# Kernel optimization log

Hardware: AMD Instinct MI355X
Metric: run time of the kernel (lower is better)

Reference implementation:

```python
import jax, jax.numpy as jnp
import numpy as np

D_MODEL = 1024
N_HEADS = 16
D_K = D_MODEL // N_HEADS
D_FF = 4096
EPS = 1e-5


def layer_norm(x, gamma, beta):
    mu = jnp.mean(x, axis=-1, keepdims=True)
    var = jnp.var(x, axis=-1, keepdims=True)
    return (x - mu) * jax.lax.rsqrt(var + EPS) * gamma + beta


def setup_inputs() -> dict:
    key = jax.random.key(0)
    ks = jax.random.split(key, 16)
    B, S = 4, 1024
    s = 0.02
    inp = {
        "x": jax.random.normal(ks[0], (B, S, D_MODEL), dtype=jnp.float32),
        "mask": jnp.ones((B, 1, 1, S), dtype=jnp.int32),
        "Wq": jax.random.normal(ks[1], (D_MODEL, D_MODEL), jnp.float32) * s,
        "bq": jnp.zeros((D_MODEL,), jnp.float32),
        "Wk": jax.random.normal(ks[2], (D_MODEL, D_MODEL), jnp.float32) * s,
        "bk": jnp.zeros((D_MODEL,), jnp.float32),
        "Wv": jax.random.normal(ks[3], (D_MODEL, D_MODEL), jnp.float32) * s,
        "bv": jnp.zeros((D_MODEL,), jnp.float32),
        "Wo": jax.random.normal(ks[4], (D_MODEL, D_MODEL), jnp.float32) * s,
        "bo": jnp.zeros((D_MODEL,), jnp.float32),
        "W1": jax.random.normal(ks[5], (D_MODEL, D_FF), jnp.float32) * s,
        "b1": jnp.zeros((D_FF,), jnp.float32),
        "W2": jax.random.normal(ks[6], (D_FF, D_MODEL), jnp.float32) * s,
        "b2": jnp.zeros((D_MODEL,), jnp.float32),
        "ln1_g": jnp.ones((D_MODEL,), jnp.float32),
        "ln1_b": jnp.zeros((D_MODEL,), jnp.float32),
        "ln2_g": jnp.ones((D_MODEL,), jnp.float32),
        "ln2_b": jnp.zeros((D_MODEL,), jnp.float32),
    }
    return inp


def reference(x, mask, Wq, bq, Wk, bk, Wv, bv, Wo, bo, W1, b1, W2, b2,
              ln1_g, ln1_b, ln2_g, ln2_b):
    B, S, _ = x.shape
    # QKV projections -> [B, H, S, d_k]
    def split_heads(t):
        return t.reshape(B, S, N_HEADS, D_K).transpose(0, 2, 1, 3)
    Q = split_heads(x @ Wq + bq)
    K = split_heads(x @ Wk + bk)
    V = split_heads(x @ Wv + bv)
    # scores [B, H, S, S]
    scores = jnp.einsum('bhqd,bhkd->bhqk', Q, K) / jnp.sqrt(jnp.float32(D_K))
    scores = jnp.where(mask == 0, jnp.float32(-1e9), scores)
    attn = jax.nn.softmax(scores, axis=-1)
    ctx = jnp.einsum('bhqk,bhkd->bhqd', attn, V)
    ctx = ctx.transpose(0, 2, 1, 3).reshape(B, S, D_MODEL)
    attn_out = ctx @ Wo + bo
    # residual + LN (dropout is identity in eval)
    h = layer_norm(x + attn_out, ln1_g, ln1_b)
    ff = jax.nn.relu(h @ W1 + b1) @ W2 + b2
    return layer_norm(h + ff, ln2_g, ln2_b)
```

## Files before the change

kernel.cpp:

```cpp
#include <hip/hip_runtime.h>
#include <hip/hip_bf16.h>

typedef __attribute__((ext_vector_type(8))) short bf16x8;
typedef __attribute__((ext_vector_type(4))) float f32x4;
typedef __attribute__((ext_vector_type(16))) float f32x16;
typedef unsigned int u32;
typedef unsigned short ush;

#define SEQ 1024
#define MTOT 4096
#define QSCALE_LOG2 0.18033688f

#if __has_builtin(__builtin_amdgcn_exp2f)
#define EXP2(x) __builtin_amdgcn_exp2f(x)
#else
#define EXP2(x) exp2f(x)
#endif

__device__ __forceinline__ ush f2bf(float f){
  u32 u = __float_as_uint(f);
  u32 r = (u + 0x7fffu + ((u >> 16) & 1u)) >> 16;
  return (ush)r;
}

__device__ __forceinline__ f32x4 mfma16(bf16x8 a, bf16x8 b, f32x4 c){
  return __builtin_amdgcn_mfma_f32_16x16x32_bf16(a, b, c, 0, 0, 0);
}
__device__ __forceinline__ f32x16 mfma32(bf16x8 a, bf16x8 b, f32x16 c){
  return __builtin_amdgcn_mfma_f32_32x32x16_bf16(a, b, c, 0, 0, 0);
}

__device__ __forceinline__ u32 cvtpk(float lo, float hi){
  u32 r; asm("v_cvt_pk_bf16_f32 %0, %1, %2" : "=v"(r) : "v"(lo), "v"(hi)); return r;
}

__device__ __forceinline__ void gload_lds16(const ush* g, ush* l){
  __builtin_amdgcn_global_load_lds(
      (const __attribute__((address_space(1))) u32*)g,
      (__attribute__((address_space(3))) u32*)l, 16, 0, 0);
}

__global__ __launch_bounds__(256) void cvt_kernel(const float* __restrict__ src,
                                                  ush* __restrict__ dst, int n){
  int i = (blockIdx.x * 256 + threadIdx.x) * 4;
  if (i < n){
    float4 v = *(const float4*)&src[i];
    ushort4 o = { f2bf(v.x), f2bf(v.y), f2bf(v.z), f2bf(v.w) };
    *(ushort4*)&dst[i] = o;
  }
}

__global__ __launch_bounds__(256) void tconv_kernel(const float* __restrict__ src,
                                                    ush* __restrict__ dst, int R, int C){
  __shared__ float t[32][33];
  int tx = threadIdx.x & 31, ty = threadIdx.x >> 5;
  int r0 = blockIdx.y * 32, c0 = blockIdx.x * 32;
  #pragma unroll
  for (int i = 0; i < 32; i += 8)
    t[ty + i][tx] = src[(size_t)(r0 + ty + i) * C + (c0 + tx)];
  __syncthreads();
  #pragma unroll
  for (int i = 0; i < 32; i += 8)
    dst[(size_t)(c0 + ty + i) * R + (r0 + tx)] = f2bf(t[tx][ty + i]);
}

__global__ __launch_bounds__(256) void biaspack_kernel(const float* __restrict__ bq,
    const float* __restrict__ bk, const float* __restrict__ bv, float* __restrict__ dst){
  int i = blockIdx.x * 256 + threadIdx.x;
  if (i < 3072){
    float v = (i < 1024) ? bq[i] : (i < 2048) ? bk[i - 1024] : bv[i - 2048];
    dst[i] = v;
  }
}

__global__ __launch_bounds__(256) void vtrans_kernel(const ush* __restrict__ qkv,
                                                     ush* __restrict__ VT){
  __shared__ ush t[32][34];
  int tx = threadIdx.x & 31, ty = threadIdx.x >> 5;
  int bh = blockIdx.z, b = bh >> 4, h = bh & 15;
  int k0 = blockIdx.x * 32, d0 = blockIdx.y * 32;
  #pragma unroll
  for (int i = 0; i < 32; i += 8)
    t[ty + i][tx] = qkv[(size_t)(b * SEQ + k0 + ty + i) * 3072 + 2048 + h * 64 + d0 + tx];
  __syncthreads();
  #pragma unroll
  for (int i = 0; i < 32; i += 8)
    VT[(size_t)(bh * 64 + d0 + ty + i) * SEQ + k0 + tx] = t[tx][ty + i];
}

__device__ __forceinline__ void stage_piece(ush* piece, const ush* g0, int K,
                                            int tid, int w){
  #pragma unroll
  for (int I = 0; I < 2; I++){
    int c = I * 512 + tid;
    int r = c >> 2;
    int gl = (c & 3) ^ ((r >> 1) & 3);
    gload_lds16(g0 + (size_t)r * K + gl * 8, piece + I * 4096 + w * 512);
  }
}

__device__ __forceinline__ bf16x8 frag(const ush* piece, int row, int g){
  int phys = g ^ ((row >> 1) & 3);
  return *(const bf16x8*)(piece + row * 32 + phys * 8);
}

#define PH_BAR_TOP() do{ __builtin_amdgcn_sched_barrier(0); \
  __builtin_amdgcn_s_barrier(); \
  asm volatile("s_waitcnt lgkmcnt(0)" ::: "memory"); \
  __builtin_amdgcn_sched_barrier(0); \
  __builtin_amdgcn_s_setprio(1); }while(0)
#define PH_BAR_BOT() do{ __builtin_amdgcn_s_setprio(0); \
  __builtin_amdgcn_sched_barrier(0); \
  __builtin_amdgcn_s_barrier(); }while(0)

template<int RELU, int OUTF32, int SCALEQ>
__global__ __launch_bounds__(512, 2) void gemm8_kernel(
    const ush* __restrict__ A, const ush* __restrict__ Bt,
    const float* __restrict__ bias,
    ush* __restrict__ Cb, float* __restrict__ Cf,
    int M, int N, int K, int ldc, int ksl)
{
  __shared__ ush lds[2][2][2][8192];
  const int tid = threadIdx.x;
  const int lane = tid & 63, w = tid >> 6;
  const int g = lane >> 4, qr = lane & 15;
  const int wr = w >> 2, wc = w & 3;
  const int gx = gridDim.x;
  const int nwg = gx * gridDim.y;
  const int id = blockIdx.y * gx + blockIdx.x;
  const int swz = (id & 7) * (nwg >> 3) + (id >> 3);
  const int bn = (swz % gx) * 256;
  const int bm = (swz / gx) * 256;
  const int kbase = blockIdx.z * ksl;
  const int NT = ksl >> 6;
  const ush* Ab = A  + (size_t)bm * K + kbase;
  const ush* Bb = Bt + (size_t)bn * K + kbase;

  stage_piece(lds[0][0][0], Ab,      K, tid, w);
  stage_piece(lds[0][1][0], Bb,      K, tid, w);
  stage_piece(lds[0][0][1], Ab + 32, K, tid, w);
  stage_piece(lds[0][1][1], Bb + 32, K, tid, w);
  if (NT > 1){
    stage_piece(lds[1][0][0], Ab + 64, K, tid, w);
    stage_piece(lds[1][1][0], Bb + 64, K, tid, w);
  }
  asm volatile("s_waitcnt vmcnt(4)" ::: "memory");
  __builtin_amdgcn_sched_barrier(0);
  __builtin_amdgcn_s_barrier();

  f32x4 acc[8][4] = {};
  const int ar = wr * 128 + qr;
  const int br = wc * 64 + qr;

  for (int T = 0; T < NT; ++T){
    const int cb = T & 1, nb = cb ^ 1;
    const ush* An = Ab + (size_t)(T + 1) * 64;
    const ush* Bn = Bb + (size_t)(T + 1) * 64;
    const ush* Af = Ab + (size_t)(T + 2) * 64;
    const ush* Bf = Bb + (size_t)(T + 2) * 64;
    bf16x8 af[4], bfr[4];

    #pragma unroll
    for (int j = 0; j < 4; j++) bfr[j] = frag(lds[cb][1][0], br + j * 16, g);
    #pragma unroll
    for (int i = 0; i < 4; i++) af[i] = frag(lds[cb][0][0], ar + i * 16, g);
    if (T + 1 < NT) stage_piece(lds[nb][0][1], An + 32, K, tid, w);
    PH_BAR_TOP();
    #pragma unroll
    for (int i = 0; i < 4; i++)
      #pragma unroll
      for (int j = 0; j < 4; j++)
        acc[i][j] = mfma16(af[i], bfr[j], acc[i][j]);
    PH_BAR_BOT();

    #pragma unroll
    for (int i = 0; i < 4; i++) af[i] = frag(lds[cb][0][0], ar + 64 + i * 16, g);
    if (T + 1 < NT) stage_piece(lds[nb][1][1], Bn + 32, K, tid, w);
    PH_BAR_TOP();
    #pragma unroll
    for (int i = 0; i < 4; i++)
      #pragma unroll
      for (int j = 0; j < 4; j++)
        acc[4 + i][j] = mfma16(af[i], bfr[j], acc[4 + i][j]);
    PH_BAR_BOT();

    #pragma unroll
    for (int j = 0; j < 4; j++) bfr[j] = frag(lds[cb][1][1], br + j * 16, g);
    #pragma unroll
    for (int i = 0; i < 4; i++) af[i] = frag(lds[cb][0][1], ar + i * 16, g);
    if (T + 2 < NT) stage_piece(lds[cb][0][0], Af, K, tid, w);
    PH_BAR_TOP();
    #pragma unroll
    for (int i = 0; i < 4; i++)
      #pragma unroll
      for (int j = 0; j < 4; j++)
        acc[i][j] = mfma16(af[i], bfr[j], acc[i][j]);
    PH_BAR_BOT();

    #pragma unroll
    for (int i = 0; i < 4; i++) af[i] = frag(lds[cb][0][1], ar + 64 + i * 16, g);
    if (T + 2 < NT) stage_piece(lds[cb][1][0], Bf, K, tid, w);
    PH_BAR_TOP();
    #pragma unroll
    for (int i = 0; i < 4; i++)
      #pragma unroll
      for (int j = 0; j < 4; j++)
        acc[4 + i][j] = mfma16(af[i], bfr[j], acc[4 + i][j]);
    __builtin_amdgcn_s_setprio(0);
    __builtin_amdgcn_sched_barrier(0);
    asm volatile("s_waitcnt vmcnt(4)" ::: "memory");
    __builtin_amdgcn_sched_barrier(0);
    __builtin_amdgcn_s_barrier();
  }

  float* Cfz = Cf;
  if (OUTF32) Cfz = Cf + (size_t)blockIdx.z * M * ldc;
  #pragma unroll
  for (int j = 0; j < 4; j++){
    const int col = bn + wc * 64 + j * 16 + qr;
    const float bv = OUTF32 ? 0.f : bias[col];
    const float scl = (SCALEQ && col < 1024) ? QSCALE_LOG2 : 1.f;
    #pragma unroll
    for (int i = 0; i < 8; i++){
      const int row0 = bm + wr * 128 + i * 16 + g * 4;
      #pragma unroll
      for (int rr = 0; rr < 4; rr++){
        float v = acc[i][j][rr] + bv;
        if (RELU) v = fmaxf(v, 0.f);
        if (SCALEQ) v *= scl;
        const size_t idx = (size_t)(row0 + rr) * ldc + col;
        if (OUTF32) Cfz[idx] = v; else Cb[idx] = f2bf(v);
      }
    }
  }
}

__global__ __launch_bounds__(256, 3) void attn2_kernel(
    const ush* __restrict__ qkv, const ush* __restrict__ VT,
    const int* __restrict__ mask, float* __restrict__ Opart,
    float* __restrict__ ml)
{
  const int tid = threadIdx.x;
  const int lane = tid & 63, w = tid >> 6;
  const int c = lane & 31, hi = lane >> 5;
  const int bh = blockIdx.z, b = bh >> 4, hh = bh & 15;
  const int split = blockIdx.y;
  const int kbeg = split * 512;
  const int q0 = blockIdx.x * 128 + w * 32;

  __shared__ int mflag;
  if (tid == 0) mflag = 1;
  __syncthreads();
  {
    int4 mv = *(const int4*)&mask[b * SEQ + tid * 4];
    if (!(mv.x && mv.y && mv.z && mv.w)) mflag = 0;
  }
  __syncthreads();
  const bool maskall = (mflag != 0);

  const ush* Qrow = qkv + (size_t)(b * SEQ + q0 + c) * 3072 + hh * 64;
  bf16x8 qf[4];
  #pragma unroll
  for (int kd = 0; kd < 4; kd++)
    qf[kd] = *(const bf16x8*)(Qrow + kd * 16 + hi * 8);

  const ush* Kb  = qkv + (size_t)(b * SEQ) * 3072 + 1024 + hh * 64;
  const ush* VTb = VT + (size_t)(bh * 64) * SEQ;

  f32x16 o0 = {}, o1 = {};
  float m_run = -1e30f, l_run = 0.f;

  bf16x8 kf[8];
  #pragma unroll
  for (int kb = 0; kb < 2; kb++)
    #pragma unroll
    for (int kd = 0; kd < 4; kd++)
      kf[kb * 4 + kd] = *(const bf16x8*)(Kb + (size_t)(kbeg + kb * 32 + c) * 3072 + kd * 16 + hi * 8);

  for (int t = 0; t < 8; ++t){
    const int k0 = kbeg + t * 64;
    bf16x8 vf[8];
    #pragma unroll
    for (int db = 0; db < 2; db++)
      #pragma unroll
      for (int ks = 0; ks < 4; ks++)
        vf[db * 4 + ks] = *(const bf16x8*)(VTb + (size_t)(db * 32 + c) * SEQ + k0 + ks * 16 + hi * 8);

    f32x16 s0 = {}, s1 = {};
    __builtin_amdgcn_s_setprio(1);
    #pragma unroll
    for (int kd = 0; kd < 4; kd++){
      s0 = mfma32(kf[kd],     qf[kd], s0);
      s1 = mfma32(kf[4 + kd], qf[kd], s1);
    }
    __builtin_amdgcn_s_setprio(0);

    float p[32];
    #pragma unroll
    for (int r = 0; r < 16; r++){ p[r] = s0[r]; p[16 + r] = s1[r]; }

    if (!maskall){
      #pragma unroll
      for (int r32 = 0; r32 < 32; r32++){
        int r = r32 & 15;
        int key = (r32 >> 4) * 32 + (r & 3) + 8 * (r >> 2) + 4 * hi;
        if (mask[b * SEQ + k0 + key] == 0) p[r32] = -1e9f;
      }
    }

    if (t + 1 < 8){
      #pragma unroll
      for (int kb = 0; kb < 2; kb++)
        #pragma unroll
        for (int kd = 0; kd < 4; kd++)
          kf[kb * 4 + kd] = *(const bf16x8*)(Kb + (size_t)(k0 + 64 + kb * 32 + c) * 3072 + kd * 16 + hi * 8);
    }

    float tm[16];
    #pragma unroll
    for (int r = 0; r < 16; r++) tm[r] = fmaxf(p[r], p[r + 16]);
    #pragma unroll
    for (int s = 8; s >= 1; s >>= 1)
      #pragma unroll
      for (int r = 0; r < s; r++) tm[r] = fmaxf(tm[r], tm[r + s]);
    float pmax = fmaxf(tm[0], __shfl_xor(tm[0], 32));

    if (__any(pmax > m_run + 8.f)){
      float m_new = fmaxf(m_run, pmax);
      float corr = EXP2(m_run - m_new);
      l_run *= corr;
      m_run = m_new;
      #pragma unroll
      for (int r = 0; r < 16; r++){
        float cr = __shfl(corr, (r & 3) + 8 * (r >> 2) + 4 * hi);
        o0[r] *= cr; o1[r] *= cr;
      }
    }

    float ts[16];
    #pragma unroll
    for (int r = 0; r < 16; r++){
      p[r]      = EXP2(p[r] - m_run);
      p[r + 16] = EXP2(p[r + 16] - m_run);
      ts[r] = p[r] + p[r + 16];
    }
    #pragma unroll
    for (int s = 8; s >= 1; s >>= 1)
      #pragma unroll
      for (int r = 0; r < s; r++) ts[r] += ts[r + s];
    l_run += ts[0] + __shfl_xor(ts[0], 32);

    union { u32 wdw[4]; bf16x8 v; } af[4];
    #pragma unroll
    for (int ks = 0; ks < 4; ks++){
      int b0 = (ks >> 1) * 16 + 8 * (ks & 1);
      u32 c00 = cvtpk(p[b0],     p[b0 + 1]);
      u32 c01 = cvtpk(p[b0 + 2], p[b0 + 3]);
      u32 c10 = cvtpk(p[b0 + 4], p[b0 + 5]);
      u32 c11 = cvtpk(p[b0 + 6], p[b0 + 7]);
      asm volatile("v_permlane32_swap_b32 %0, %1" : "+v"(c10), "+v"(c00));
      asm volatile("v_permlane32_swap_b32 %0, %1" : "+v"(c11), "+v"(c01));
      af[ks].wdw[0] = c00; af[ks].wdw[1] = c01; af[ks].wdw[2] = c10; af[ks].wdw[3] = c11;
    }

    __builtin_amdgcn_s_setprio(1);
    #pragma unroll
    for (int ks = 0; ks < 4; ks++){
      o0 = mfma32(af[ks].v, vf[ks],     o0);
      o1 = mfma32(af[ks].v, vf[4 + ks], o1);
    }
    __builtin_amdgcn_s_setprio(0);
  }

  if (lane < 32){
    float2* mlp = (float2*)ml;
    mlp[((size_t)split * 64 + bh) * SEQ + q0 + c] = make_float2(m_run, l_run);
  }
  #pragma unroll
  for (int r = 0; r < 16; r++){
    int crow = (r & 3) + 8 * (r >> 2) + 4 * hi;
    size_t base = (size_t)split * MTOT * 1024 + (size_t)(b * SEQ + q0 + crow) * 1024 + hh * 64;
    Opart[base + c]      = o0[r];
    Opart[base + 32 + c] = o1[r];
  }
}

__global__ __launch_bounds__(256) void attn_combine_kernel(
    const float* __restrict__ Opart, const float* __restrict__ ml,
    ush* __restrict__ ctx)
{
  const int row = blockIdx.x;
  const int b = row >> 10, q = row & 1023;
  const int col = threadIdx.x * 4;
  const int hh = col >> 6;
  const int bh = b * 16 + hh;
  const float2* mlp = (const float2*)ml;
  float2 a0 = mlp[(size_t)bh * SEQ + q];
  float2 a1 = mlp[((size_t)64 + bh) * SEQ + q];
  float m = fmaxf(a0.x, a1.x);
  float w0 = EXP2(a0.x - m), w1 = EXP2(a1.x - m);
  float li = 1.f / fmaxf(a0.y * w0 + a1.y * w1, 1e-30f);
  size_t base = (size_t)row * 1024 + col;
  float4 u = *(const float4*)&Opart[base];
  float4 v = *(const float4*)&Opart[(size_t)MTOT * 1024 + base];
  ushort4 o;
  o.x = f2bf((u.x * w0 + v.x * w1) * li);
  o.y = f2bf((u.y * w0 + v.y * w1) * li);
  o.z = f2bf((u.z * w0 + v.z * w1) * li);
  o.w = f2bf((u.w * w0 + v.w * w1) * li);
  *(ushort4*)&ctx[base] = o;
}

template<bool WB>
__global__ __launch_bounds__(256) void ln4_kernel(
    const float* __restrict__ X, const float* __restrict__ P,
    const float* __restrict__ bias,
    const float* __restrict__ gam, const float* __restrict__ bet,
    float* __restrict__ Of, ush* __restrict__ Ob)
{
  const int row = blockIdx.x, tid = threadIdx.x;
  const size_t base = (size_t)row * 1024 + tid * 4;
  float4 xv = *(const float4*)&X[base];
  float4 bv4 = *(const float4*)&bias[tid * 4];
  float s0 = xv.x + bv4.x, s1 = xv.y + bv4.y, s2 = xv.z + bv4.z, s3 = xv.w + bv4.w;
  #pragma unroll
  for (int z = 0; z < 4; z++){
    float4 p = *(const float4*)&P[(size_t)z * 4194304 + base];
    s0 += p.x; s1 += p.y; s2 += p.z; s3 += p.w;
  }
  float sum = s0 + s1 + s2 + s3;
  float sq  = s0 * s0 + s1 * s1 + s2 * s2 + s3 * s3;
  #pragma unroll
  for (int o = 1; o < 64; o <<= 1){ sum += __shfl_xor(sum, o); sq += __shfl_xor(sq, o); }
  __shared__ float red[8];
  int lane = tid & 63, w = tid >> 6;
  if (lane == 0){ red[w] = sum; red[4 + w] = sq; }
  __syncthreads();
  sum = red[0] + red[1] + red[2] + red[3];
  sq  = red[4] + red[5] + red[6] + red[7];
  float mean = sum * (1.f / 1024.f);
  float var  = sq * (1.f / 1024.f) - mean * mean;
  float rs = rsqrtf(var + 1e-5f);
  float4 gv = *(const float4*)&gam[tid * 4];
  float4 bt = *(const float4*)&bet[tid * 4];
  float o0 = (s0 - mean) * rs * gv.x + bt.x;
  float o1 = (s1 - mean) * rs * gv.y + bt.y;
  float o2 = (s2 - mean) * rs * gv.z + bt.z;
  float o3 = (s3 - mean) * rs * gv.w + bt.w;
  float4 ov = { o0, o1, o2, o3 };
  *(float4*)&Of[base] = ov;
  if (WB){
    ushort4 ob = { f2bf(o0), f2bf(o1), f2bf(o2), f2bf(o3) };
    *(ushort4*)&Ob[base] = ob;
  }
}

extern "C" void kernel_launch(void* const* d_in, const int* in_sizes, int n_in,
                              void* d_out, int out_size, void* d_ws, size_t ws_size,
                              hipStream_t stream)
{
  const float* x    = (const float*)d_in[0];
  const int*   mask = (const int*)  d_in[1];
  const float* Wq = (const float*)d_in[2];
  const float* bq = (const float*)d_in[3];
  const float* Wk = (const float*)d_in[4];
  const float* bk = (const float*)d_in[5];
  const float* Wv = (const float*)d_in[6];
  const float* bv = (const float*)d_in[7];
  const float* Wo = (const float*)d_in[8];
  const float* bo = (const float*)d_in[9];
  const float* W1 = (const float*)d_in[10];
  const float* b1 = (const float*)d_in[11];
  const float* W2 = (const float*)d_in[12];
  const float* b2 = (const float*)d_in[13];
  const float* g1 = (const float*)d_in[14];
  const float* be1= (const float*)d_in[15];
  const float* g2 = (const float*)d_in[16];
  const float* be2= (const float*)d_in[17];
  float* out = (float*)d_out;

  char* ws = (char*)d_ws;
  size_t off = 0;
  auto alloc = [&](size_t bytes)->void*{ void* p = ws + off; off += (bytes + 255) & ~(size_t)255; return p; };
  ush* xb     = (ush*)alloc((size_t)MTOT * 1024 * 2);
  ush* wqkvT  = (ush*)alloc((size_t)3072 * 1024 * 2);
  ush* woT    = (ush*)alloc((size_t)1024 * 1024 * 2);
  ush* w1T    = (ush*)alloc((size_t)4096 * 1024 * 2);
  ush* w2T    = (ush*)alloc((size_t)1024 * 4096 * 2);
  float* bqkv = (float*)alloc(3072 * 4);
  ush* qkv    = (ush*)alloc((size_t)MTOT * 3072 * 2);
  ush* ctx    = (ush*)alloc((size_t)MTOT * 1024 * 2);
  float* part = (float*)alloc((size_t)4 * MTOT * 1024 * 4);
  float* h    = (float*)alloc((size_t)MTOT * 1024 * 4);
  ush* hb     = (ush*)alloc((size_t)MTOT * 1024 * 2);
  ush* VT     = (ush*)alloc((size_t)64 * 64 * SEQ * 2);
  ush* ff1    = qkv;
  float* Opart = part;
  float* mlbuf = part + (size_t)2 * MTOT * 1024;

  cvt_kernel<<<dim3(4096), dim3(256), 0, stream>>>(x, xb, MTOT * 1024);
  tconv_kernel<<<dim3(32, 32), dim3(256), 0, stream>>>(Wq, wqkvT,               1024, 1024);
  tconv_kernel<<<dim3(32, 32), dim3(256), 0, stream>>>(Wk, wqkvT + 1024 * 1024, 1024, 1024);
  tconv_kernel<<<dim3(32, 32), dim3(256), 0, stream>>>(Wv, wqkvT + 2048 * 1024, 1024, 1024);
  tconv_kernel<<<dim3(32, 32), dim3(256), 0, stream>>>(Wo, woT,                 1024, 1024);
  tconv_kernel<<<dim3(128, 32), dim3(256), 0, stream>>>(W1, w1T, 1024, 4096);
  tconv_kernel<<<dim3(32, 128), dim3(256), 0, stream>>>(W2, w2T, 4096, 1024);
  biaspack_kernel<<<dim3(12), dim3(256), 0, stream>>>(bq, bk, bv, bqkv);

  gemm8_kernel<0, 0, 1><<<dim3(12, 16, 1), dim3(512), 0, stream>>>(
      xb, wqkvT, bqkv, qkv, nullptr, MTOT, 3072, 1024, 3072, 1024);

  vtrans_kernel<<<dim3(32, 2, 64), dim3(256), 0, stream>>>(qkv, VT);

  attn2_kernel<<<dim3(8, 2, 64), dim3(256), 0, stream>>>(qkv, VT, mask, Opart, mlbuf);
  attn_combine_kernel<<<dim3(4096), dim3(256), 0, stream>>>(Opart, mlbuf, ctx);

  gemm8_kernel<0, 1, 0><<<dim3(4, 16, 4), dim3(512), 0, stream>>>(
      ctx, woT, nullptr, nullptr, part, MTOT, 1024, 1024, 1024, 256);

  ln4_kernel<true><<<dim3(4096), dim3(256), 0, stream>>>(x, part, bo, g1, be1, h, hb);

  gemm8_kernel<1, 0, 0><<<dim3(16, 16, 1), dim3(512), 0, stream>>>(
      hb, w1T, b1, ff1, nullptr, MTOT, 4096, 1024, 4096, 1024);

  gemm8_kernel<0, 1, 0><<<dim3(4, 16, 4), dim3(512), 0, stream>>>(
      ff1, w2T, nullptr, nullptr, part, MTOT, 1024, 4096, 1024, 1024);

  ln4_kernel<false><<<dim3(4096), dim3(256), 0, stream>>>(h, part, b2, g2, be2, out, nullptr);
}
```

Baseline: 419.8 us.

## Fuse split-K attention combine into attention kernel via shared memory

Each block now holds two query groups, each split over two key halves handled by separate waves. The partial outputs and running max/sum go to shared memory and are merged in-kernel before writing bf16 context directly. This removes the fp32 partial-output round trip through global memory and the separate combine launch. The cost is about 35KB of LDS per block and the loss of the occupancy hint of 3 blocks, which may reduce occupancy.

```diff
diff --git a/kernel.cpp b/kernel.cpp
--- a/kernel.cpp
+++ b/kernel.cpp
@@ -235,20 +235,22 @@
   }
 }
 
-__global__ __launch_bounds__(256, 3) void attn2_kernel(
+__global__ __launch_bounds__(256) void attn2_kernel(
     const ush* __restrict__ qkv, const ush* __restrict__ VT,
-    const int* __restrict__ mask, float* __restrict__ Opart,
-    float* __restrict__ ml)
+    const int* __restrict__ mask, ush* __restrict__ ctx)
 {
+  __shared__ float Ocomb[2][2][32][68];
+  __shared__ float mlsh[2][2][2][32];
+  __shared__ int mflag;
+
   const int tid = threadIdx.x;
   const int lane = tid & 63, w = tid >> 6;
   const int c = lane & 31, hi = lane >> 5;
-  const int bh = blockIdx.z, b = bh >> 4, hh = bh & 15;
-  const int split = blockIdx.y;
-  const int kbeg = split * 512;
-  const int q0 = blockIdx.x * 128 + w * 32;
-
-  __shared__ int mflag;
+  const int wq = w >> 1, ws = w & 1;
+  const int bh = blockIdx.y, b = bh >> 4, hh = bh & 15;
+  const int kbeg = ws * 512;
+  const int q0 = blockIdx.x * 64 + wq * 32;
+
   if (tid == 0) mflag = 1;
   __syncthreads();
   {
@@ -373,42 +375,38 @@
   }
 
   if (lane < 32){
-    float2* mlp = (float2*)ml;
-    mlp[((size_t)split * 64 + bh) * SEQ + q0 + c] = make_float2(m_run, l_run);
+    mlsh[wq][ws][0][c] = m_run;
+    mlsh[wq][ws][1][c] = l_run;
   }
   #pragma unroll
   for (int r = 0; r < 16; r++){
     int crow = (r & 3) + 8 * (r >> 2) + 4 * hi;
-    size_t base = (size_t)split * MTOT * 1024 + (size_t)(b * SEQ + q0 + crow) * 1024 + hh * 64;
-    Opart[base + c]      = o0[r];
-    Opart[base + 32 + c] = o1[r];
-  }
-}
-
-__global__ __launch_bounds__(256) void attn_combine_kernel(
-    const float* __restrict__ Opart, const float* __restrict__ ml,
-    ush* __restrict__ ctx)
-{
-  const int row = blockIdx.x;
-  const int b = row >> 10, q = row & 1023;
-  const int col = threadIdx.x * 4;
-  const int hh = col >> 6;
-  const int bh = b * 16 + hh;
-  const float2* mlp = (const float2*)ml;
-  float2 a0 = mlp[(size_t)bh * SEQ + q];
-  float2 a1 = mlp[((size_t)64 + bh) * SEQ + q];
-  float m = fmaxf(a0.x, a1.x);
-  float w0 = EXP2(a0.x - m), w1 = EXP2(a1.x - m);
-  float li = 1.f / fmaxf(a0.y * w0 + a1.y * w1, 1e-30f);
-  size_t base = (size_t)row * 1024 + col;
-  float4 u = *(const float4*)&Opart[base];
-  float4 v = *(const float4*)&Opart[(size_t)MTOT * 1024 + base];
-  ushort4 o;
-  o.x = f2bf((u.x * w0 + v.x * w1) * li);
-  o.y = f2bf((u.y * w0 + v.y * w1) * li);
-  o.z = f2bf((u.z * w0 + v.z * w1) * li);
-  o.w = f2bf((u.w * w0 + v.w * w1) * li);
-  *(ushort4*)&ctx[base] = o;
+    Ocomb[wq][ws][crow][c]      = o0[r];
+    Ocomb[wq][ws][crow][32 + c] = o1[r];
+  }
+  __syncthreads();
+
+  {
+    const int r2 = c;
+    const int cbase = ws * 32 + hi * 16;
+    float m0 = mlsh[wq][0][0][r2], l0 = mlsh[wq][0][1][r2];
+    float m1 = mlsh[wq][1][0][r2], l1 = mlsh[wq][1][1][r2];
+    float m  = fmaxf(m0, m1);
+    float w0 = EXP2(m0 - m), w1 = EXP2(m1 - m);
+    float li = 1.f / fmaxf(l0 * w0 + l1 * w1, 1e-30f);
+    size_t gbase = (size_t)(b * SEQ + q0 + r2) * 1024 + hh * 64 + cbase;
+    #pragma unroll
+    for (int cc = 0; cc < 16; cc += 4){
+      float4 u = *(const float4*)&Ocomb[wq][0][r2][cbase + cc];
+      float4 v = *(const float4*)&Ocomb[wq][1][r2][cbase + cc];
+      ushort4 ob;
+      ob.x = f2bf((u.x * w0 + v.x * w1) * li);
+      ob.y = f2bf((u.y * w0 + v.y * w1) * li);
+      ob.z = f2bf((u.z * w0 + v.z * w1) * li);
+      ob.w = f2bf((u.w * w0 + v.w * w1) * li);
+      *(ushort4*)&ctx[gbase + cc] = ob;
+    }
+  }
 }
 
 template<bool WB>
@@ -495,8 +493,6 @@
   ush* hb     = (ush*)alloc((size_t)MTOT * 1024 * 2);
   ush* VT     = (ush*)alloc((size_t)64 * 64 * SEQ * 2);
   ush* ff1    = qkv;
-  float* Opart = part;
-  float* mlbuf = part + (size_t)2 * MTOT * 1024;
 
   cvt_kernel<<<dim3(4096), dim3(256), 0, stream>>>(x, xb, MTOT * 1024);
   tconv_kernel<<<dim3(32, 32), dim3(256), 0, stream>>>(Wq, wqkvT,               1024, 1024);
@@ -512,8 +508,7 @@
 
   vtrans_kernel<<<dim3(32, 2, 64), dim3(256), 0, stream>>>(qkv, VT);
 
-  attn2_kernel<<<dim3(8, 2, 64), dim3(256), 0, stream>>>(qkv, VT, mask, Opart, mlbuf);
-  attn_combine_kernel<<<dim3(4096), dim3(256), 0, stream>>>(Opart, mlbuf, ctx);
+  attn2_kernel<<<dim3(16, 64), dim3(256), 0, stream>>>(qkv, VT, mask, ctx);
 
   gemm8_kernel<0, 1, 0><<<dim3(4, 16, 4), dim3(512), 0, stream>>>(
       ctx, woT, nullptr, nullptr, part, MTOT, 1024, 1024, 1024, 256);
```

Measured after the change: 395.7 us. -5.7%, faster.
